# Optimization experiments

Measured on AMD Instinct MI355X. Metric: run time of the kernel, lower is better.

## Reference

```python
import jax, jax.numpy as jnp
import numpy as np

B, S, D = 8, 4096, 1024
F = 4 * D  # expert hidden dim (internal_dim = d_model * 4)
E = 8      # num experts


def setup_inputs() -> dict:
    key = jax.random.key(0)
    ks = jax.random.split(key, 7)
    x = jax.random.normal(ks[0], (B, S, D), dtype=jnp.float32)
    expert_weights = jax.random.uniform(ks[1], (B, 1), dtype=jnp.float32)
    expert_indices = jax.random.randint(ks[2], (B, 1), 0, E)
    # Per-expert MLP params: Linear(D,F) -> GELU -> Linear(F,D)
    W1 = jax.random.normal(ks[3], (E, D, F), dtype=jnp.float32) / np.sqrt(D)
    b1 = jnp.zeros((E, F), dtype=jnp.float32)
    W2 = jax.random.normal(ks[4], (E, F, D), dtype=jnp.float32) / np.sqrt(F)
    b2 = jnp.zeros((E, D), dtype=jnp.float32)
    return {"x": x, "expert_weights": expert_weights, "W1": W1, "b1": b1,
            "W2": W2, "b2": b2, "expert_indices": expert_indices}


def reference(x, expert_weights, W1, b1, W2, b2, expert_indices):
    # Top-1 routing per sequence (router built with top_k=1):
    # each batch element b is processed by expert idx[b], output scaled by w[b].
    idx = expert_indices[:, 0]          # [B]
    w = expert_weights[:, 0]            # [B]
    w1 = W1[idx]                        # [B, D, F] gather of expert params
    w2 = W2[idx]                        # [B, F, D]
    h = jnp.einsum('bsd,bdf->bsf', x, w1) + b1[idx][:, None, :]
    h = jax.nn.gelu(h, approximate=False)  # torch nn.GELU default = exact erf
    y = jnp.einsum('bsf,bfd->bsd', h, w2) + b2[idx][:, None, :]
    # weighted scatter-combine: final_output[mask] += expert_output * w
    return y * w[:, None, None]
```

## Files before the change

### kernel.cpp

```cpp
#include <hip/hip_runtime.h>
#include <hip/hip_bf16.h>


#define B_ 8
#define S_ 4096
#define D_ 1024
#define F_ 4096
#define E_ 8

typedef __bf16 bf16x8 __attribute__((ext_vector_type(8)));
typedef float f32x4 __attribute__((ext_vector_type(4)));

__device__ __forceinline__ unsigned short f2bf(float f) {
  unsigned u = __float_as_uint(f);
  u += 0x7FFFu + ((u >> 16) & 1u);
  return (unsigned short)(u >> 16);
}

#define GLD16(g, l) __builtin_amdgcn_global_load_lds(                         \
    (const __attribute__((address_space(1))) unsigned int*)(g),              \
    (__attribute__((address_space(3))) unsigned int*)(l), 16, 0, 0)

__global__ __launch_bounds__(256) void transpose_cvt_kernel(
    const float* __restrict__ src, unsigned short* __restrict__ dst,
    int R, int C) {
  __shared__ float t[32][33];
  const float* s = src + (size_t)blockIdx.z * R * C;
  unsigned short* d = dst + (size_t)blockIdx.z * R * C;
  int c0 = blockIdx.x * 32, r0 = blockIdx.y * 32;
  int x = threadIdx.x, y = threadIdx.y;
#pragma unroll
  for (int j = 0; j < 32; j += 8)
    t[y + j][x] = s[(size_t)(r0 + y + j) * C + (c0 + x)];
  __syncthreads();
#pragma unroll
  for (int j = 0; j < 32; j += 8)
    d[(size_t)(c0 + y + j) * R + (r0 + x)] = f2bf(t[x][y + j]);
}

__global__ __launch_bounds__(256) void cvt_bf16_kernel(
    const float* __restrict__ src, unsigned short* __restrict__ dst, long n4) {
  long i = (long)blockIdx.x * 256 + threadIdx.x;
  long stride = (long)gridDim.x * 256;
  for (; i < n4; i += stride) {
    float4 v = ((const float4*)src)[i];
    uint2 o;
    o.x = (unsigned)f2bf(v.x) | ((unsigned)f2bf(v.y) << 16);
    o.y = (unsigned)f2bf(v.z) | ((unsigned)f2bf(v.w) << 16);
    ((uint2*)dst)[i] = o;
  }
}


#define STAGE(cur, op, h, tk, base)                                           \
  {                                                                           \
    const unsigned short* g0_ = (base) + (size_t)((h) * 128 + sr) * LDK +     \
                                (tk) * 64 + sgc * 8;                          \
    GLD16(g0_, smem + (cur) * 65536 + (op) * 32768 + (h) * 16384 +            \
                   wave * 1024);                                              \
    GLD16(g0_ + (size_t)64 * LDK,                                             \
          smem + (cur) * 65536 + (op) * 32768 + (h) * 16384 + 8192 +          \
              wave * 1024);                                                   \
  }

#define LDA_HALF(cur, H)                                                      \
  _Pragma("unroll") for (int m = 0; m < 4; ++m) {                             \
    const char* p_ = smem + (cur) * 65536 + (H) * 16384 +                     \
                     (wr * 64 + m * 16 + l15) * 128;                          \
    aM[m][0] = *(const bf16x8*)(p_ + ca0);                                    \
    aM[m][1] = *(const bf16x8*)(p_ + ca1);                                    \
  }

#define LDB_Q(cur, Q, breg)                                                   \
  _Pragma("unroll") for (int n = 0; n < 2; ++n) {                             \
    const char* p_ = smem + (cur) * 65536 + 32768 + (Q) * 16384 +             \
                     (wc * 32 + n * 16 + l15) * 128;                          \
    breg[n][0] = *(const bf16x8*)(p_ + ca0);                                  \
    breg[n][1] = *(const bf16x8*)(p_ + ca1);                                  \
  }

#define MMA_Q(MB, breg, NB)                                                   \
  _Pragma("unroll") for (int ks = 0; ks < 2; ++ks)                            \
      _Pragma("unroll") for (int m = 0; m < 4; ++m)                           \
          _Pragma("unroll") for (int n = 0; n < 2; ++n)                       \
              acc[(MB) + m][(NB) + n] =                                       \
      __builtin_amdgcn_mfma_f32_16x16x32_bf16(                                \
          aM[m][ks], breg[n][ks], acc[(MB) + m][(NB) + n], 0, 0, 0);

#define PH_END                                                                \
  __builtin_amdgcn_s_setprio(0);                                              \
  __builtin_amdgcn_sched_barrier(0);                                          \
  __builtin_amdgcn_s_barrier();

#define TILE(cur, t, MODE)                                                    \
  LDA_HALF(cur, 0);                                                           \
  LDB_Q(cur, 0, bq0);                                                         \
  if ((MODE) >= 1) STAGE((cur) ^ 1, 0, 1, (t) + 1, Abase);                    \
  __builtin_amdgcn_s_setprio(1);                                              \
  MMA_Q(0, bq0, 0);                                                           \
  PH_END;                                                                     \
  LDB_Q(cur, 1, bq1);                                                         \
  if ((MODE) == 2) STAGE(cur, 0, 0, (t) + 2, Abase);                          \
  __builtin_amdgcn_s_setprio(1);                                              \
  MMA_Q(0, bq1, 2);                                                           \
  PH_END;                                                                     \
  LDA_HALF(cur, 1);                                                           \
  if ((MODE) == 2) STAGE(cur, 1, 0, (t) + 2, Bbase);                          \
  __builtin_amdgcn_s_setprio(1);                                              \
  MMA_Q(4, bq0, 0);                                                           \
  PH_END;                                                                     \
  if ((MODE) == 2) STAGE(cur, 1, 1, (t) + 2, Bbase);                          \
  __builtin_amdgcn_s_setprio(1);                                              \
  MMA_Q(4, bq1, 2);                                                           \
  __builtin_amdgcn_s_setprio(0);                                              \
  __builtin_amdgcn_sched_barrier(0);                                          \
  if ((MODE) == 2) asm volatile("s_waitcnt vmcnt(6)" ::: "memory");           \
  if ((MODE) == 1) asm volatile("s_waitcnt vmcnt(0)" ::: "memory");           \
  __builtin_amdgcn_s_barrier();

template <int NT, int LDK, int NCOL, bool GELU>
__global__ __launch_bounds__(512, 2) void gemm8p_kernel(
    const unsigned short* __restrict__ A,
    const unsigned short* __restrict__ Bw,
    const float* __restrict__ bias,
    const int* __restrict__ eidx, const float* __restrict__ ew,
    void* __restrict__ Out, int grow0, int nbm) {
  extern __shared__ __align__(16) char smem[];

  const int tid = threadIdx.x;
  const int lane = tid & 63;
  const int wave = tid >> 6;
  const int wr = wave >> 2;
  const int wc = wave & 3;
  const int l15 = lane & 15, lhi = lane >> 4;

  const int nwg = nbm * (NCOL / 256);
  int wg = blockIdx.x;
  if ((nwg & 7) == 0) wg = (wg & 7) * (nwg >> 3) + (wg >> 3);
  const int bm = wg % nbm, bn = wg / nbm;

  const int bat = (grow0 + bm * 256) >> 12;
  const int e = eidx[bat];

  const unsigned short* Abase = A + (size_t)bm * 256 * LDK;
  const unsigned short* Bbase =
      Bw + (size_t)e * (F_ * D_) + (size_t)bn * 256 * LDK;

  const int sr = tid >> 3;
  const int sgc = (tid & 7) ^ (sr & 7);
  const int ca0 = ((lhi ^ (l15 & 7)) << 4);
  const int ca1 = (((4 + lhi) ^ (l15 & 7)) << 4);

  f32x4 acc[8][4] = {};
  bf16x8 aM[4][2], bq0[2][2], bq1[2][2];

  STAGE(0, 0, 0, 0, Abase);
  STAGE(0, 1, 0, 0, Bbase);
  STAGE(0, 1, 1, 0, Bbase);
  STAGE(0, 0, 1, 0, Abase);
  STAGE(1, 0, 0, 1, Abase);
  STAGE(1, 1, 0, 1, Bbase);
  STAGE(1, 1, 1, 1, Bbase);
  asm volatile("s_waitcnt vmcnt(6)" ::: "memory");
  __builtin_amdgcn_s_barrier();

#pragma unroll 1
  for (int t = 0; t < NT - 2; t += 2) {
    TILE(0, t, 2);
    TILE(1, t + 1, 2);
  }
  TILE(0, NT - 2, 1);
  TILE(1, NT - 1, 0);

  const float scale = GELU ? 1.0f : ew[bat];
#pragma unroll
  for (int n = 0; n < 4; ++n) {
    const int tcol =
        (n < 2 ? wc * 32 + n * 16 : 128 + wc * 32 + (n - 2) * 16) + l15;
    const int col = bn * 256 + tcol;
    const float bv = bias[(size_t)e * NCOL + col];
#pragma unroll
    for (int m = 0; m < 8; ++m) {
      const int trow =
          (m < 4 ? wr * 64 + m * 16 : 128 + wr * 64 + (m - 4) * 16) + lhi * 4;
      const size_t rowb = (size_t)bm * 256 + trow;
#pragma unroll
      for (int r = 0; r < 4; ++r) {
        float v = acc[m][n][r] + bv;
        if (GELU) {
          float zz = v * (0.79788456080286536f + 0.0356774081f * v * v);
          float g = v / (1.0f + __expf(-2.0f * zz));
          ((unsigned short*)Out)[(rowb + r) * NCOL + col] = f2bf(g);
        } else {
          ((float*)Out)[(rowb + r) * NCOL + col] = v * scale;
        }
      }
    }
  }
}

extern "C" void kernel_launch(void* const* d_in, const int* in_sizes, int n_in,
                              void* d_out, int out_size, void* d_ws,
                              size_t ws_size, hipStream_t stream) {
  const float* x = (const float*)d_in[0];
  const float* ew = (const float*)d_in[1];
  const float* W1 = (const float*)d_in[2];
  const float* b1 = (const float*)d_in[3];
  const float* W2 = (const float*)d_in[4];
  const float* b2 = (const float*)d_in[5];
  const int* eidx = (const int*)d_in[6];
  float* out = (float*)d_out;

  char* ws = (char*)d_ws;
  const size_t WT = (size_t)E_ * F_ * D_ * 2;
  const size_t XB = (size_t)B_ * S_ * D_ * 2;
  unsigned short* w1t = (unsigned short*)ws;
  unsigned short* w2t = (unsigned short*)(ws + WT);

  auto g1 = gemm8p_kernel<16, D_, F_, true>;
  auto g2 = gemm8p_kernel<64, F_, D_, false>;
  hipFuncSetAttribute((const void*)g1,
                      hipFuncAttributeMaxDynamicSharedMemorySize, 131072);
  hipFuncSetAttribute((const void*)g2,
                      hipFuncAttributeMaxDynamicSharedMemorySize, 131072);

  transpose_cvt_kernel<<<dim3(F_ / 32, D_ / 32, E_), dim3(32, 8), 0, stream>>>(
      W1, w1t, D_, F_);
  transpose_cvt_kernel<<<dim3(D_ / 32, F_ / 32, E_), dim3(32, 8), 0, stream>>>(
      W2, w2t, F_, D_);

  const long total_rows = (long)B_ * S_;
  long hcap = ((long)ws_size - (long)(2 * WT + XB)) / ((long)F_ * 2);

  if (hcap >= total_rows) {
    unsigned short* xbf = (unsigned short*)(ws + 2 * WT);
    unsigned short* hbuf = (unsigned short*)(ws + 2 * WT + XB);
    cvt_bf16_kernel<<<2048, 256, 0, stream>>>(x, xbf, (long)B_ * S_ * D_ / 4);
    int nbm = (int)(total_rows / 256);
    g1<<<dim3(nbm * (F_ / 256)), 512, 131072, stream>>>(
        xbf, w1t, b1, eidx, ew, hbuf, 0, nbm);
    g2<<<dim3(nbm * (D_ / 256)), 512, 131072, stream>>>(
        hbuf, w2t, b2, eidx, ew, out, 0, nbm);
  } else {
    long cap = ((long)ws_size - (long)(2 * WT)) / ((long)(D_ + F_) * 2);
    long chunk = (cap / 256) * 256;
    if (chunk > total_rows) chunk = total_rows;
    if (chunk < 256) chunk = 256;
    unsigned short* xbf = (unsigned short*)(ws + 2 * WT);
    unsigned short* hbuf = xbf + (size_t)chunk * D_;
    for (long r0 = 0; r0 < total_rows; r0 += chunk) {
      long nr = total_rows - r0;
      if (nr > chunk) nr = chunk;
      cvt_bf16_kernel<<<512, 256, 0, stream>>>(x + r0 * D_, xbf, nr * D_ / 4);
      int nbm = (int)(nr / 256);
      g1<<<dim3(nbm * (F_ / 256)), 512, 131072, stream>>>(
          xbf, w1t, b1, eidx, ew, hbuf, (int)r0, nbm);
      g2<<<dim3(nbm * (D_ / 256)), 512, 131072, stream>>>(
          hbuf, w2t, b2, eidx, ew, out + r0 * D_, (int)r0, nbm);
    }
  }
}
```

Baseline: 708.6 us.

## Replace phased multi-stage GEMM pipeline with simple double-buffered prefetch

Drops the four-phase schedule that refilled the current LDS buffer for tile t+2 between MFMA quarters. That schedule relied on per-phase workgroup barriers, s_setprio hints and partial vmcnt waits. The new code issues all global-to-LDS loads for tile t+1 at the top of each tile, runs all MFMA quarters, then waits for vmcnt(0) and a single barrier. This removes three barriers per tile and the priority toggling. The cost is a shallower prefetch, since only one tile is in flight, and a full memory drain every tile, which may expose global-load latency.

```diff
diff --git a/kernel.cpp b/kernel.cpp
--- a/kernel.cpp
+++ b/kernel.cpp
@@ -87,36 +87,25 @@
       __builtin_amdgcn_mfma_f32_16x16x32_bf16(                                \
           aM[m][ks], breg[n][ks], acc[(MB) + m][(NB) + n], 0, 0, 0);
 
-#define PH_END                                                                \
-  __builtin_amdgcn_s_setprio(0);                                              \
-  __builtin_amdgcn_sched_barrier(0);                                          \
-  __builtin_amdgcn_s_barrier();
-
 #define TILE(cur, t, MODE)                                                    \
+  if ((MODE) >= 1) {                                                          \
+    STAGE((cur) ^ 1, 0, 0, (t) + 1, Abase);                                   \
+    STAGE((cur) ^ 1, 1, 0, (t) + 1, Bbase);                                   \
+    STAGE((cur) ^ 1, 0, 1, (t) + 1, Abase);                                   \
+    STAGE((cur) ^ 1, 1, 1, (t) + 1, Bbase);                                   \
+  }                                                                           \
   LDA_HALF(cur, 0);                                                           \
   LDB_Q(cur, 0, bq0);                                                         \
-  if ((MODE) >= 1) STAGE((cur) ^ 1, 0, 1, (t) + 1, Abase);                    \
-  __builtin_amdgcn_s_setprio(1);                                              \
+  LDB_Q(cur, 1, bq1);                                                         \
   MMA_Q(0, bq0, 0);                                                           \
-  PH_END;                                                                     \
-  LDB_Q(cur, 1, bq1);                                                         \
-  if ((MODE) == 2) STAGE(cur, 0, 0, (t) + 2, Abase);                          \
-  __builtin_amdgcn_s_setprio(1);                                              \
   MMA_Q(0, bq1, 2);                                                           \
-  PH_END;                                                                     \
   LDA_HALF(cur, 1);                                                           \
-  if ((MODE) == 2) STAGE(cur, 1, 0, (t) + 2, Bbase);                          \
-  __builtin_amdgcn_s_setprio(1);                                              \
   MMA_Q(4, bq0, 0);                                                           \
-  PH_END;                                                                     \
-  if ((MODE) == 2) STAGE(cur, 1, 1, (t) + 2, Bbase);                          \
-  __builtin_amdgcn_s_setprio(1);                                              \
   MMA_Q(4, bq1, 2);                                                           \
-  __builtin_amdgcn_s_setprio(0);                                              \
-  __builtin_amdgcn_sched_barrier(0);                                          \
-  if ((MODE) == 2) asm volatile("s_waitcnt vmcnt(6)" ::: "memory");           \
-  if ((MODE) == 1) asm volatile("s_waitcnt vmcnt(0)" ::: "memory");           \
-  __builtin_amdgcn_s_barrier();
+  if ((MODE) >= 1) {                                                          \
+    asm volatile("s_waitcnt vmcnt(0)" ::: "memory");                          \
+    __builtin_amdgcn_s_barrier();                                             \
+  }
 
 template <int NT, int LDK, int NCOL, bool GELU>
 __global__ __launch_bounds__(512, 2) void gemm8p_kernel(
@@ -156,18 +145,15 @@
 
   STAGE(0, 0, 0, 0, Abase);
   STAGE(0, 1, 0, 0, Bbase);
+  STAGE(0, 0, 1, 0, Abase);
   STAGE(0, 1, 1, 0, Bbase);
-  STAGE(0, 0, 1, 0, Abase);
-  STAGE(1, 0, 0, 1, Abase);
-  STAGE(1, 1, 0, 1, Bbase);
-  STAGE(1, 1, 1, 1, Bbase);
-  asm volatile("s_waitcnt vmcnt(6)" ::: "memory");
+  asm volatile("s_waitcnt vmcnt(0)" ::: "memory");
   __builtin_amdgcn_s_barrier();
 
 #pragma unroll 1
   for (int t = 0; t < NT - 2; t += 2) {
-    TILE(0, t, 2);
-    TILE(1, t + 1, 2);
+    TILE(0, t, 1);
+    TILE(1, t + 1, 1);
   }
   TILE(0, NT - 2, 1);
   TILE(1, NT - 1, 0);
```

After: 824.5 us. +16.4%, slower.

## Stage GELU output through LDS for coalesced stores and chunk rows for L2 reuse

Applied to the files above, without the earlier changes.

The first GEMM's GELU epilogue now writes bf16 results into shared memory and then copies them out with 16-byte row-contiguous stores, replacing scattered 2-byte global writes. The host loop also splits the rows into chunks of up to 16384, so the intermediate H buffer is smaller and more likely to stay in cache between the two GEMMs. The cost is two extra barriers and an LDS round trip per tile, plus more kernel launches.

```diff
diff --git a/kernel.cpp b/kernel.cpp
--- a/kernel.cpp
+++ b/kernel.cpp
@@ -172,28 +172,55 @@
   TILE(0, NT - 2, 1);
   TILE(1, NT - 1, 0);
 
-  const float scale = GELU ? 1.0f : ew[bat];
-#pragma unroll
-  for (int n = 0; n < 4; ++n) {
-    const int tcol =
-        (n < 2 ? wc * 32 + n * 16 : 128 + wc * 32 + (n - 2) * 16) + l15;
-    const int col = bn * 256 + tcol;
-    const float bv = bias[(size_t)e * NCOL + col];
-#pragma unroll
-    for (int m = 0; m < 8; ++m) {
-      const int trow =
-          (m < 4 ? wr * 64 + m * 16 : 128 + wr * 64 + (m - 4) * 16) + lhi * 4;
-      const size_t rowb = (size_t)bm * 256 + trow;
-#pragma unroll
-      for (int r = 0; r < 4; ++r) {
-        float v = acc[m][n][r] + bv;
-        if (GELU) {
+  if (GELU) {
+    __builtin_amdgcn_s_barrier();
+    unsigned short* cs = (unsigned short*)smem;
+#pragma unroll
+    for (int n = 0; n < 4; ++n) {
+      const int tcol =
+          (n < 2 ? wc * 32 + n * 16 : 128 + wc * 32 + (n - 2) * 16) + l15;
+      const float bv = bias[(size_t)e * NCOL + bn * 256 + tcol];
+#pragma unroll
+      for (int m = 0; m < 8; ++m) {
+        const int trow =
+            (m < 4 ? wr * 64 + m * 16 : 128 + wr * 64 + (m - 4) * 16) +
+            lhi * 4;
+#pragma unroll
+        for (int r = 0; r < 4; ++r) {
+          float v = acc[m][n][r] + bv;
           float zz = v * (0.79788456080286536f + 0.0356774081f * v * v);
           float g = v / (1.0f + __expf(-2.0f * zz));
-          ((unsigned short*)Out)[(rowb + r) * NCOL + col] = f2bf(g);
-        } else {
-          ((float*)Out)[(rowb + r) * NCOL + col] = v * scale;
+          cs[(trow + r) * 256 + tcol] = f2bf(g);
         }
+      }
+    }
+    __builtin_amdgcn_s_barrier();
+    unsigned short* Hо = (unsigned short*)Out + (size_t)bm * 256 * NCOL +
+                         (size_t)bn * 256;
+    const int rsub = tid >> 5, cc = tid & 31;
+#pragma unroll
+    for (int it = 0; it < 16; ++it) {
+      const int row = it * 16 + rsub;
+      *(uint4*)(Hо + (size_t)row * NCOL + cc * 8) =
+          *(const uint4*)(smem + row * 512 + cc * 16);
+    }
+  } else {
+    const float scale = ew[bat];
+#pragma unroll
+    for (int n = 0; n < 4; ++n) {
+      const int tcol =
+          (n < 2 ? wc * 32 + n * 16 : 128 + wc * 32 + (n - 2) * 16) + l15;
+      const int col = bn * 256 + tcol;
+      const float bv = bias[(size_t)e * NCOL + col];
+#pragma unroll
+      for (int m = 0; m < 8; ++m) {
+        const int trow =
+            (m < 4 ? wr * 64 + m * 16 : 128 + wr * 64 + (m - 4) * 16) +
+            lhi * 4;
+        const size_t rowb = (size_t)bm * 256 + trow;
+#pragma unroll
+        for (int r = 0; r < 4; ++r)
+          ((float*)Out)[(rowb + r) * NCOL + col] = (acc[m][n][r] + bv) * scale;
       }
     }
   }
@@ -230,17 +257,26 @@
       W2, w2t, F_, D_);
 
   const long total_rows = (long)B_ * S_;
-  long hcap = ((long)ws_size - (long)(2 * WT + XB)) / ((long)F_ * 2);
-
-  if (hcap >= total_rows) {
+
+  long avail = (long)ws_size - (long)(2 * WT + XB);
+  long CH = avail > 0 ? (avail / ((long)F_ * 2)) : 0;
+  CH = (CH / 256) * 256;
+  if (CH > 16384) CH = 16384;
+  if (CH > total_rows) CH = total_rows;
+
+  if (CH >= 256) {
     unsigned short* xbf = (unsigned short*)(ws + 2 * WT);
     unsigned short* hbuf = (unsigned short*)(ws + 2 * WT + XB);
     cvt_bf16_kernel<<<2048, 256, 0, stream>>>(x, xbf, (long)B_ * S_ * D_ / 4);
-    int nbm = (int)(total_rows / 256);
-    g1<<<dim3(nbm * (F_ / 256)), 512, 131072, stream>>>(
-        xbf, w1t, b1, eidx, ew, hbuf, 0, nbm);
-    g2<<<dim3(nbm * (D_ / 256)), 512, 131072, stream>>>(
-        hbuf, w2t, b2, eidx, ew, out, 0, nbm);
+    for (long r0 = 0; r0 < total_rows; r0 += CH) {
+      long nr = total_rows - r0;
+      if (nr > CH) nr = CH;
+      int nbm = (int)(nr / 256);
+      g1<<<dim3(nbm * (F_ / 256)), 512, 131072, stream>>>(
+          xbf + r0 * D_, w1t, b1, eidx, ew, hbuf, (int)r0, nbm);
+      g2<<<dim3(nbm * (D_ / 256)), 512, 131072, stream>>>(
+          hbuf, w2t, b2, eidx, ew, out + r0 * D_, (int)r0, nbm);
+    }
   } else {
     long cap = ((long)ws_size - (long)(2 * WT)) / ((long)(D_ + F_) * 2);
     long chunk = (cap / 256) * 256;
```

Result: no change. 698.1 us (-1.5%).

## Chunk GEMM pair into 16K-row slices and remap B-tile columns per wave

Applied to the files above, without the earlier changes.

The host now splits the rows into chunks of at most 16384 and runs the two GEMMs alternately per chunk. The intent is to keep the intermediate H buffer small enough to stay resident in the last-level cache between the first and second GEMM, instead of writing all of H to HBM and reading it back. Inside the kernel, each wave's N columns are remapped to a contiguous 64-column block, so the epilogue hoists the bias loads and writes four columns per row in a tighter pattern. The trade-off is extra kernel launches and smaller grids per launch, which may lower occupancy at the tail of each chunk.

```diff
diff --git a/kernel.cpp b/kernel.cpp
--- a/kernel.cpp
+++ b/kernel.cpp
@@ -73,8 +73,8 @@
 
 #define LDB_Q(cur, Q, breg)                                                   \
   _Pragma("unroll") for (int n = 0; n < 2; ++n) {                             \
-    const char* p_ = smem + (cur) * 65536 + 32768 + (Q) * 16384 +             \
-                     (wc * 32 + n * 16 + l15) * 128;                          \
+    const char* p_ = smem + (cur) * 65536 + 32768 + (wc >> 1) * 16384 +       \
+                     ((wc & 1) * 64 + ((Q) * 2 + n) * 16 + l15) * 128;        \
     breg[n][0] = *(const bf16x8*)(p_ + ca0);                                  \
     breg[n][1] = *(const bf16x8*)(p_ + ca1);                                  \
   }
@@ -172,28 +172,32 @@
   TILE(0, NT - 2, 1);
   TILE(1, NT - 1, 0);
 
+  const int colbase = bn * 256 + (wc >> 1) * 128 + (wc & 1) * 64 + l15;
+  float bv[4];
+#pragma unroll
+  for (int n = 0; n < 4; ++n) bv[n] = bias[(size_t)e * NCOL + colbase + n * 16];
   const float scale = GELU ? 1.0f : ew[bat];
-#pragma unroll
-  for (int n = 0; n < 4; ++n) {
-    const int tcol =
-        (n < 2 ? wc * 32 + n * 16 : 128 + wc * 32 + (n - 2) * 16) + l15;
-    const int col = bn * 256 + tcol;
-    const float bv = bias[(size_t)e * NCOL + col];
-#pragma unroll
-    for (int m = 0; m < 8; ++m) {
-      const int trow =
-          (m < 4 ? wr * 64 + m * 16 : 128 + wr * 64 + (m - 4) * 16) + lhi * 4;
-      const size_t rowb = (size_t)bm * 256 + trow;
-#pragma unroll
-      for (int r = 0; r < 4; ++r) {
-        float v = acc[m][n][r] + bv;
-        if (GELU) {
+
+#pragma unroll
+  for (int m = 0; m < 8; ++m) {
+    const int trow =
+        (m < 4 ? wr * 64 + m * 16 : 128 + wr * 64 + (m - 4) * 16) + lhi * 4;
+    const size_t rowb = (size_t)bm * 256 + trow;
+#pragma unroll
+    for (int r = 0; r < 4; ++r) {
+      const size_t off = (rowb + r) * NCOL + colbase;
+      if (GELU) {
+#pragma unroll
+        for (int n = 0; n < 4; ++n) {
+          float v = acc[m][n][r] + bv[n];
           float zz = v * (0.79788456080286536f + 0.0356774081f * v * v);
           float g = v / (1.0f + __expf(-2.0f * zz));
-          ((unsigned short*)Out)[(rowb + r) * NCOL + col] = f2bf(g);
-        } else {
-          ((float*)Out)[(rowb + r) * NCOL + col] = v * scale;
+          ((unsigned short*)Out)[off + n * 16] = f2bf(g);
         }
+      } else {
+#pragma unroll
+        for (int n = 0; n < 4; ++n)
+          ((float*)Out)[off + n * 16] = (acc[m][n][r] + bv[n]) * scale;
       }
     }
   }
@@ -230,17 +234,26 @@
       W2, w2t, F_, D_);
 
   const long total_rows = (long)B_ * S_;
-  long hcap = ((long)ws_size - (long)(2 * WT + XB)) / ((long)F_ * 2);
-
-  if (hcap >= total_rows) {
+
+  long avail = (long)ws_size - (long)(2 * WT + XB);
+  long CH = avail > 0 ? (avail / ((long)F_ * 2)) : 0;
+  CH = (CH / 256) * 256;
+  if (CH > 16384) CH = 16384;
+  if (CH > total_rows) CH = total_rows;
+
+  if (CH >= 256) {
     unsigned short* xbf = (unsigned short*)(ws + 2 * WT);
     unsigned short* hbuf = (unsigned short*)(ws + 2 * WT + XB);
     cvt_bf16_kernel<<<2048, 256, 0, stream>>>(x, xbf, (long)B_ * S_ * D_ / 4);
-    int nbm = (int)(total_rows / 256);
-    g1<<<dim3(nbm * (F_ / 256)), 512, 131072, stream>>>(
-        xbf, w1t, b1, eidx, ew, hbuf, 0, nbm);
-    g2<<<dim3(nbm * (D_ / 256)), 512, 131072, stream>>>(
-        hbuf, w2t, b2, eidx, ew, out, 0, nbm);
+    for (long r0 = 0; r0 < total_rows; r0 += CH) {
+      long nr = total_rows - r0;
+      if (nr > CH) nr = CH;
+      int nbm = (int)(nr / 256);
+      g1<<<dim3(nbm * (F_ / 256)), 512, 131072, stream>>>(
+          xbf + r0 * D_, w1t, b1, eidx, ew, hbuf, (int)r0, nbm);
+      g2<<<dim3(nbm * (D_ / 256)), 512, 131072, stream>>>(
+          hbuf, w2t, b2, eidx, ew, out + r0 * D_, (int)r0, nbm);
+    }
   } else {
     long cap = ((long)ws_size - (long)(2 * WT)) / ((long)(D_ + F_) * 2);
     long chunk = (cap / 256) * 256;
```

Measured after the change: 663.2 us. 6.4% less time.
